# Kernel optimization log

Hardware: AMD Instinct MI355X
Metric: run time of the kernel (lower is better)

## Reference

```python
import jax, jax.numpy as jnp
import numpy as np
from jax import lax

DIM = 512
DH = 16          # dim_head
H = DIM // DH    # 32 heads
WS = 7           # window_size
SR = 3           # sr_ratio (AvgPool2d kernel, stride=1)
EPS = 1e-5


def _rel_pos_indices():
    # mirrors the torch buffer construction, incl. the [:, 24:] slice for sr_ratio>1
    pos = np.arange(WS)
    gi, gj = np.meshgrid(pos, pos, indexing='ij')
    grid = np.stack([gi, gj], axis=-1).reshape(-1, 2)            # (49, 2)
    rel = grid[:, None, :] - grid[None, :, :] + (WS - 1)         # (49, 49, 2)
    idx = rel[..., 0] * (2 * WS - 1) + rel[..., 1]               # (49, 49)
    return jnp.asarray(idx[:, 24:], dtype=jnp.int32)             # (49, 25)


def _layernorm(x, g, b):
    m = jnp.mean(x, axis=-1, keepdims=True)
    v = jnp.mean(jnp.square(x - m), axis=-1, keepdims=True)
    return (x - m) * lax.rsqrt(v + EPS) * g + b


def setup_inputs() -> dict:
    key = jax.random.key(0)
    ks = jax.random.split(key, 8)
    B, X, Y = 8, 14, 14
    x = jax.random.normal(ks[0], (B, X, Y, WS, WS, DIM), dtype=jnp.float32)
    ln_gamma = 1.0 + 0.1 * jax.random.normal(ks[1], (DIM,), dtype=jnp.float32)
    ln_beta = 0.1 * jax.random.normal(ks[2], (DIM,), dtype=jnp.float32)
    s = 1.0 / np.sqrt(DIM)
    Wq = jax.random.normal(ks[3], (DIM, DIM), dtype=jnp.float32) * s
    Wkv = jax.random.normal(ks[4], (2 * DIM, DIM), dtype=jnp.float32) * s
    Wout = jax.random.normal(ks[5], (DIM, DIM), dtype=jnp.float32) * s
    rel_pos_emb = 0.02 * jax.random.normal(ks[6], ((2 * WS - 1) ** 2, H), dtype=jnp.float32)
    return {"x": x, "ln_gamma": ln_gamma, "ln_beta": ln_beta,
            "Wq": Wq, "Wkv": Wkv, "Wout": Wout, "rel_pos_emb": rel_pos_emb}


def reference(x, ln_gamma, ln_beta, Wq, Wkv, Wout, rel_pos_emb):
    B, X, Y, W1, W2, D = x.shape
    Nw = B * X * Y                      # number of windows
    Nq = W1 * W2                        # 49 query tokens per window
    xn = _layernorm(x, ln_gamma, ln_beta)
    xw = xn.reshape(Nw, Nq, D)
    # queries
    q = (xw @ Wq.T).reshape(Nw, Nq, H, DH).transpose(0, 2, 1, 3) * (DH ** -0.5)  # (Nw,H,Nq,DH)
    # KV spatial reduction: AvgPool2d(kernel=SR, stride=1) over the 7x7 window
    xi = xw.reshape(Nw, W1, W2, D)
    xp = lax.reduce_window(xi, 0.0, lax.add, (1, SR, SR, 1), (1, 1, 1, 1), 'VALID') / (SR * SR)
    Hp, Wp = W1 - SR + 1, W2 - SR + 1   # 5, 5
    xkv = _layernorm(xp.reshape(Nw, Hp * Wp, D), ln_gamma, ln_beta)
    # to_kv with einops '(dim h l)' decomposition: last axis factored as (DH, H, 2)
    kv = (xkv @ Wkv.T).reshape(Nw, Hp * Wp, DH, H, 2)
    k = kv[..., 0].transpose(0, 3, 1, 2)  # (Nw, H, Nk, DH)
    v = kv[..., 1].transpose(0, 3, 1, 2)
    sim = jnp.einsum('bhid,bhjd->bhij', q, k)                    # (Nw,H,49,25)
    bias = rel_pos_emb[_rel_pos_indices()]                       # (49,25,H)
    sim = sim + bias.transpose(2, 0, 1)[None]
    attn = jax.nn.softmax(sim, axis=-1)
    out = jnp.einsum('bhij,bhjd->bhid', attn, v)                 # (Nw,H,49,DH)
    out = out.reshape(Nw, H, W1, W2, DH).transpose(0, 2, 3, 1, 4).reshape(Nw, W1, W2, D)
    out = out @ Wout.T
    return out.reshape(B, X, Y, W1, W2, D)
```

## Files before the change

### kernel.cpp

```cpp
#include <hip/hip_runtime.h>

typedef _Float16 half8 __attribute__((ext_vector_type(8)));
typedef _Float16 half4 __attribute__((ext_vector_type(4)));
typedef float f32x4 __attribute__((ext_vector_type(4)));

#define MFMA16(a,b,c) __builtin_amdgcn_mfma_f32_16x16x32_f16(a,b,c,0,0,0)
#define GLOAD16(g, l) __builtin_amdgcn_global_load_lds( \
  (const __attribute__((address_space(1))) void*)(g), \
  (__attribute__((address_space(3))) void*)(l), 16, 0, 0)
#define SCHEDB() __builtin_amdgcn_sched_barrier(0)

static constexpr int NW     = 1568;
static constexpr int MROWSQ = 76832;
static constexpr int MPADQ  = 76928;
static constexpr int MROWKV = 39200;
static constexpr int MPADKV = 39296;
static constexpr float LOG2E = 1.4426950408889634f;

__device__ __forceinline__ half8 h8z(){
  half8 z = {(_Float16)0,(_Float16)0,(_Float16)0,(_Float16)0,
             (_Float16)0,(_Float16)0,(_Float16)0,(_Float16)0};
  return z;
}

__global__ void k_prep_w(const float* __restrict__ a, const float* __restrict__ b,
                         const float* __restrict__ c,
                         _Float16* __restrict__ ah, _Float16* __restrict__ bh,
                         _Float16* __restrict__ ch){
  int i = blockIdx.x*256 + threadIdx.x;
  if(i < 262144) ah[i] = (_Float16)(a[i]*(0.25f*LOG2E));
  int j = i - 262144;
  if(j >= 0 && j < 524288) bh[j] = (_Float16)b[j];
  int k = i - 786432;
  if(k >= 0 && k < 262144) ch[k] = (_Float16)c[k];
}

__global__ void k_prep_bias(const float* __restrict__ rel, float* __restrict__ biasT){
  int t = blockIdx.x*256 + threadIdx.x;
  if(t >= 65536) return;
  int h = t >> 11;
  int r = t & 2047;
  int i = r >> 5, slotk = r & 31;
  int kg = slotk >> 3, idx = slotk & 7;
  int j = (idx < 4) ? (kg*4 + idx) : (16 + kg*4 + idx - 4);
  float v = 0.f;
  if(j >= 25) v = -1e30f;
  else if(i < 49){
    int qi = i/7, qj = i%7;
    int c = j + 24, ki = c/7, kj = c%7;
    v = rel[((qi-ki+6)*13 + (qj-kj+6))*32 + h];
  }
  biasT[t] = v*LOG2E;
}

__global__ __launch_bounds__(512) void k_ln_pool(const float* __restrict__ x,
    const float* __restrict__ gamma, const float* __restrict__ beta,
    _Float16* __restrict__ xn, _Float16* __restrict__ xkv){
  __shared__ _Float16 nrm[49*512];
  const int w = blockIdx.x, t = threadIdx.x;
  const int lane = t & 63, wv = t >> 6;
  float gf[8], bf[8];
  {
    float4 g0 = *(const float4*)(gamma + lane*8);
    float4 g1 = *(const float4*)(gamma + lane*8 + 4);
    float4 b0 = *(const float4*)(beta  + lane*8);
    float4 b1 = *(const float4*)(beta  + lane*8 + 4);
    gf[0]=g0.x; gf[1]=g0.y; gf[2]=g0.z; gf[3]=g0.w;
    gf[4]=g1.x; gf[5]=g1.y; gf[6]=g1.z; gf[7]=g1.w;
    bf[0]=b0.x; bf[1]=b0.y; bf[2]=b0.z; bf[3]=b0.w;
    bf[4]=b1.x; bf[5]=b1.y; bf[6]=b1.z; bf[7]=b1.w;
  }
  const float* xw = x + (size_t)w*49*512;
  for(int i = wv; i < 49; i += 8){
    const float* row = xw + i*512 + lane*8;
    float4 v0 = *(const float4*)row;
    float4 v1 = *(const float4*)(row+4);
    float v[8] = {v0.x,v0.y,v0.z,v0.w,v1.x,v1.y,v1.z,v1.w};
    float s = 0.f, sq = 0.f;
    #pragma unroll
    for(int j=0;j<8;j++){ s += v[j]; sq += v[j]*v[j]; }
    #pragma unroll
    for(int o=32;o>=1;o>>=1){ s += __shfl_xor(s,o); sq += __shfl_xor(sq,o); }
    float mean = s*(1.f/512.f);
    float rstd = rsqrtf(sq*(1.f/512.f) - mean*mean + 1e-5f);
    half8 nh;
    #pragma unroll
    for(int j=0;j<8;j++)
      nh[j] = (_Float16)((v[j]-mean)*rstd*gf[j] + bf[j]);
    *(half8*)&nrm[i*512 + lane*8] = nh;
    *(half8*)(xn + ((size_t)w*49 + i)*512 + lane*8) = nh;
  }
  __syncthreads();
  for(int p = wv; p < 25; p += 8){
    const int pi = p/5, pj = p%5;
    float acc[8] = {0,0,0,0,0,0,0,0};
    #pragma unroll
    for(int a=0;a<3;a++)
      #pragma unroll
      for(int bb=0;bb<3;bb++){
        half8 rv = *(const half8*)&nrm[((pi+a)*7 + (pj+bb))*512 + lane*8];
        #pragma unroll
        for(int j=0;j<8;j++) acc[j] += (float)rv[j];
      }
    float s = 0.f, sq = 0.f;
    #pragma unroll
    for(int j=0;j<8;j++){ acc[j] *= (1.f/9.f); s += acc[j]; sq += acc[j]*acc[j]; }
    #pragma unroll
    for(int o=32;o>=1;o>>=1){ s += __shfl_xor(s,o); sq += __shfl_xor(sq,o); }
    float mean = s*(1.f/512.f);
    float rstd = rsqrtf(sq*(1.f/512.f) - mean*mean + 1e-5f);
    half8 nh;
    #pragma unroll
    for(int j=0;j<8;j++) nh[j] = (_Float16)((acc[j]-mean)*rstd*gf[j] + bf[j]);
    *(half8*)(xkv + ((size_t)w*25 + p)*512 + lane*8) = nh;
  }
}

template<int MODE>
__global__ __launch_bounds__(256) void k_gemm(const _Float16* __restrict__ A,
    const _Float16* __restrict__ Bw, _Float16* __restrict__ oh,
    float* __restrict__ of, int ldc, int ntn, int nwg){
  __shared__ __align__(16) _Float16 As[3][128*32];
  __shared__ __align__(16) _Float16 Bs[3][128*32];
  const int orig = blockIdx.x;
  const int xcd = orig & 7, slot = orig >> 3;
  const int q8 = nwg >> 3, r8 = nwg & 7;
  const int base = (xcd < r8) ? xcd*(q8+1) : r8*(q8+1) + (xcd-r8)*q8;
  const int lin = base + slot;
  const int m0 = (lin / ntn) * 128, n0 = (lin % ntn) * 128;
  const int t = threadIdx.x, lane = t & 63;
  const int wid = t >> 6, wm = (wid>>1)*64, wn = (wid&1)*64;
  const int lr = lane & 15, kg = lane >> 4;
  const _Float16* Ab = A  + (size_t)m0*512;
  const _Float16* Bb = Bw + (size_t)n0*512;
  const int foff0 = wid*64, foff1 = 256 + wid*64;
  const int f0 = foff0 + lane, f1 = foff1 + lane;
  const int r0 = f0 >> 2, r1 = f1 >> 2;
  const size_t ga0 = (size_t)r0*512 + ((f0&3) ^ ((r0>>1)&3))*8;
  const size_t ga1 = (size_t)r1*512 + ((f1&3) ^ ((r1>>1)&3))*8;
  const int swz = (lr>>1) & 3;

  auto STAGE = [&](int buf, int kt){
    const int k0 = kt*32;
    GLOAD16(Ab + ga0 + k0, &As[buf][foff0*8]);
    GLOAD16(Bb + ga0 + k0, &Bs[buf][foff0*8]);
    GLOAD16(Ab + ga1 + k0, &As[buf][foff1*8]);
    GLOAD16(Bb + ga1 + k0, &Bs[buf][foff1*8]);
  };
  STAGE(0, 0);
  STAGE(1, 1);

  f32x4 acc[4][4] = {};
  int buf = 0;
  for(int kt = 0; kt < 16; ++kt){
    if(kt + 2 < 16){
      int nb = buf + 2; if(nb >= 3) nb -= 3;
      STAGE(nb, kt + 2);
    }
    if(kt < 14)       asm volatile("s_waitcnt vmcnt(8)" ::: "memory");
    else if(kt == 14) asm volatile("s_waitcnt vmcnt(4)" ::: "memory");
    else              asm volatile("s_waitcnt vmcnt(0)" ::: "memory");
    SCHEDB();
    __builtin_amdgcn_s_barrier();
    SCHEDB();
    const _Float16* Ac = As[buf];
    const _Float16* Bc = Bs[buf];
    half8 af[4], bf[4];
    #pragma unroll
    for(int mt=0;mt<4;mt++)
      af[mt] = *(const half8*)&Ac[(wm + mt*16 + lr)*32 + (kg ^ swz)*8];
    #pragma unroll
    for(int nt=0;nt<4;nt++)
      bf[nt] = *(const half8*)&Bc[(wn + nt*16 + lr)*32 + (kg ^ swz)*8];
    #pragma unroll
    for(int mt=0;mt<4;mt++)
      #pragma unroll
      for(int nt=0;nt<4;nt++)
        acc[mt][nt] = MFMA16(af[mt], bf[nt], acc[mt][nt]);
    SCHEDB();
    __builtin_amdgcn_s_barrier();
    SCHEDB();
    buf += 1; if(buf >= 3) buf -= 3;
  }
  #pragma unroll
  for(int mt=0;mt<4;mt++)
    #pragma unroll
    for(int nt=0;nt<4;nt++)
      #pragma unroll
      for(int r=0;r<4;r++){
        int row = m0 + wm + mt*16 + kg*4 + r;
        int col = n0 + wn + nt*16 + lr;
        float vv = acc[mt][nt][r];
        if(MODE == 0){
          oh[(size_t)row*ldc + col] = (_Float16)vv;
        } else {
          if(row < MROWSQ) of[(size_t)row*ldc + col] = vv;
        }
      }
}

__global__ __launch_bounds__(256) void k_repack(const _Float16* __restrict__ kvb,
    _Float16* __restrict__ kb, _Float16* __restrict__ vb){
  __shared__ uint2 s2[6400];
  uint32_t* su = (uint32_t*)s2;
  const int w = blockIdx.x, t = threadIdx.x;
  const uint2* src = (const uint2*)(kvb + (size_t)w*25*1024);
  #pragma unroll
  for(int it=0; it<25; ++it){
    int U = it*256 + t;
    int j = U >> 8, u = U & 255;
    s2[j*256 + (u ^ (u>>4) ^ (j&15))] = src[U];
  }
  __syncthreads();
  _Float16* kdst = kb + (size_t)w*12800;
  for(int it=0; it<7; ++it){
    int q = it*256 + t;
    if(q < 1600){
      int h = q/50, rem = q%50, j = rem>>1, half = rem&1;
      half8 k8;
      #pragma unroll
      for(int jj=0;jj<8;jj++){
        int dh = half*8 + jj;
        int slot = j*256 + ((dh*16 + (h>>1)) ^ dh ^ (j&15));
        uint32_t val = su[slot*2 + (h&1)];
        k8[jj] = ((_Float16*)&val)[0];
      }
      *(half8*)(kdst + q*8) = k8;
    }
  }
  _Float16* vtdst = vb + (size_t)w*16384;
  for(int it=0; it<8; ++it){
    int u = it*256 + t;
    int h = u >> 6, rem = u & 63;
    int dh = rem >> 2, jq = rem & 3;
    half8 v8 = h8z();
    #pragma unroll
    for(int jj=0;jj<8;jj++){
      int j = jq*8 + jj;
      if(j < 25){
        int slot = j*256 + ((dh*16 + (h>>1)) ^ dh ^ (j&15));
        uint32_t val = su[slot*2 + (h&1)];
        v8[jj] = ((_Float16*)&val)[1];
      }
    }
    *(half8*)(vtdst + u*8) = v8;
  }
}

__global__ __launch_bounds__(256) void k_attn(const _Float16* __restrict__ q,
    const _Float16* __restrict__ kb, const _Float16* __restrict__ vb,
    const float* __restrict__ biasT, _Float16* __restrict__ ao){
  const int w = blockIdx.x, hi = blockIdx.y, t = threadIdx.x;
  const int lane = t & 63, wv = t >> 6;
  const int lr = lane & 15, kg = lane >> 4;
  const size_t qbase = ((size_t)w*49)*512;
  const int hA = hi*4 + wv;
  const size_t kvA = (((size_t)w*32 + hA)*25)*16;
  const size_t kvB = kvA + 6400;
  half8 kA0=h8z(), kA1=h8z(), kB0=h8z(), kB1=h8z();
  if(kg < 2){
    kA0 = *(const half8*)(kb + kvA + lr*16 + kg*8);
    kB0 = *(const half8*)(kb + kvB + lr*16 + kg*8);
    if(lr < 9){
      kA1 = *(const half8*)(kb + kvA + (16+lr)*16 + kg*8);
      kB1 = *(const half8*)(kb + kvB + (16+lr)*16 + kg*8);
    }
  }
  half8 qA[4], qB[4];
  #pragma unroll
  for(int qt=0;qt<4;qt++){
    if(kg < 2){
      const _Float16* p = q + qbase + (size_t)(qt*16+lr)*512 + hA*16 + kg*8;
      qA[qt] = *(const half8*)p;
      qB[qt] = *(const half8*)(p + 256);
    } else { qA[qt] = h8z(); qB[qt] = h8z(); }
  }
  half8 vA, vB;
  {
    const _Float16* vtA = vb + ((size_t)w*32 + hA)*512 + lr*32 + kg*4;
    const _Float16* vtB = vtA + 16*512;
    half4 a0 = *(const half4*)vtA;
    half4 a1 = *(const half4*)(vtA + 16);
    half4 b0 = *(const half4*)vtB;
    half4 b1 = *(const half4*)(vtB + 16);
    vA = __builtin_shufflevector(a0, a1, 0,1,2,3,4,5,6,7);
    vB = __builtin_shufflevector(b0, b1, 0,1,2,3,4,5,6,7);
  }
  const float4* btA = (const float4*)(biasT + (size_t)hA*2048);
  const float4* btB = (const float4*)(biasT + (size_t)(hA+16)*2048);
  #pragma unroll
  for(int qt=0;qt<4;qt++){
    f32x4 sA0={}, sA1={}, sB0={}, sB1={};
    sA0 = MFMA16(kA0, qA[qt], sA0);
    sA1 = MFMA16(kA1, qA[qt], sA1);
    sB0 = MFMA16(kB0, qB[qt], sB0);
    sB1 = MFMA16(kB1, qB[qt], sB1);
    const int i = qt*16 + lr;
    const int bidx = i*8 + kg*2;
    float4 bA0 = btA[bidx], bA1 = btA[bidx+1];
    float4 bB0 = btB[bidx], bB1 = btB[bidx+1];
    float a[8], b[8];
    a[0]=sA0[0]+bA0.x; a[1]=sA0[1]+bA0.y; a[2]=sA0[2]+bA0.z; a[3]=sA0[3]+bA0.w;
    a[4]=sA1[0]+bA1.x; a[5]=sA1[1]+bA1.y; a[6]=sA1[2]+bA1.z; a[7]=sA1[3]+bA1.w;
    b[0]=sB0[0]+bB0.x; b[1]=sB0[1]+bB0.y; b[2]=sB0[2]+bB0.z; b[3]=sB0[3]+bB0.w;
    b[4]=sB1[0]+bB1.x; b[5]=sB1[1]+bB1.y; b[6]=sB1[2]+bB1.z; b[7]=sB1[3]+bB1.w;
    float mA = a[0], mB = b[0];
    #pragma unroll
    for(int j=1;j<8;j++){ mA = fmaxf(mA, a[j]); mB = fmaxf(mB, b[j]); }
    mA = fmaxf(mA, __shfl_xor(mA,16)); mB = fmaxf(mB, __shfl_xor(mB,16));
    mA = fmaxf(mA, __shfl_xor(mA,32)); mB = fmaxf(mB, __shfl_xor(mB,32));
    float sumA = 0.f, sumB = 0.f;
    #pragma unroll
    for(int j=0;j<8;j++){
      a[j] = exp2f(a[j]-mA); sumA += a[j];
      b[j] = exp2f(b[j]-mB); sumB += b[j];
    }
    sumA += __shfl_xor(sumA,16); sumB += __shfl_xor(sumB,16);
    sumA += __shfl_xor(sumA,32); sumB += __shfl_xor(sumB,32);
    float invA = 1.f/sumA, invB = 1.f/sumB;
    half8 pA, pB;
    #pragma unroll
    for(int j=0;j<8;j++){
      pA[j] = (_Float16)(a[j]*invA);
      pB[j] = (_Float16)(b[j]*invB);
    }
    f32x4 oA={}, oB={};
    oA = MFMA16(pA, vA, oA);
    oB = MFMA16(pB, vB, oB);
    #pragma unroll
    for(int r=0;r<4;r++){
      int qi2 = qt*16 + kg*4 + r;
      if(qi2 < 49){
        _Float16* dst = ao + qbase + (size_t)qi2*512 + hA*16 + lr;
        dst[0]   = (_Float16)oA[r];
        dst[256] = (_Float16)oB[r];
      }
    }
  }
}

extern "C" void kernel_launch(void* const* d_in, const int* in_sizes, int n_in,
                              void* d_out, int out_size, void* d_ws, size_t ws_size,
                              hipStream_t stream){
  (void)in_sizes; (void)n_in; (void)out_size; (void)ws_size;
  const float* x    = (const float*)d_in[0];
  const float* gam  = (const float*)d_in[1];
  const float* bet  = (const float*)d_in[2];
  const float* Wq   = (const float*)d_in[3];
  const float* Wkv  = (const float*)d_in[4];
  const float* Wout = (const float*)d_in[5];
  const float* rel  = (const float*)d_in[6];
  float* out = (float*)d_out;

  char* ws = (char*)d_ws;
  size_t off = 0;
  auto alloc = [&](size_t n){ char* p = ws + off; off += (n + 1023) & ~(size_t)1023; return p; };
  _Float16* xn    = (_Float16*)alloc((size_t)MPADQ*512*2);
  _Float16* xkv   = (_Float16*)alloc((size_t)MPADKV*512*2);
  _Float16* kvb   = (_Float16*)alloc((size_t)MPADKV*1024*2);
  _Float16* kbuf  = (_Float16*)alloc((size_t)NW*32*25*16*2);
  _Float16* vbuf  = (_Float16*)alloc((size_t)NW*32*16*32*2);
  _Float16* wqh   = (_Float16*)alloc((size_t)262144*2);
  _Float16* wkvh  = (_Float16*)alloc((size_t)524288*2);
  _Float16* wouth = (_Float16*)alloc((size_t)262144*2);
  float*    biasT = (float*)   alloc((size_t)65536*4);
  _Float16* qb    = kvb;

  k_prep_w   <<<dim3(4096), 256, 0, stream>>>(Wq, Wkv, Wout, wqh, wkvh, wouth);
  k_prep_bias<<<dim3(256),  256, 0, stream>>>(rel, biasT);
  k_ln_pool  <<<dim3(NW),   512, 0, stream>>>(x, gam, bet, xn, xkv);
  k_gemm<0>  <<<dim3(2456), 256, 0, stream>>>(xkv, wkvh, kvb, nullptr, 1024, 8, 2456);
  k_repack   <<<dim3(NW),   256, 0, stream>>>(kvb, kbuf, vbuf);
  k_gemm<0>  <<<dim3(2404), 256, 0, stream>>>(xn,  wqh,  qb,  nullptr,  512, 4, 2404);
  k_attn     <<<dim3(NW,4), 256, 0, stream>>>(qb, kbuf, vbuf, biasT, xn);
  k_gemm<1>  <<<dim3(2404), 256, 0, stream>>>(xn,  wouth, nullptr, out, 512, 4, 2404);
}
```

Baseline: 385.5 us.

## Process four heads per wave in attention and two rows per iteration in LN

The attention kernel now has each wave handle four heads (strided by 8) instead of two, which halves the grid's y dimension. Q fragments are loaded per query tile inside the loop rather than all being preloaded. The LN/pool kernel processes two rows or pooled positions per wave iteration to expose more independent memory loads and shuffle reductions. These changes aim to raise instruction-level parallelism and amortise per-block overhead, at the cost of more registers and fewer blocks.

```diff
diff --git a/kernel.cpp b/kernel.cpp
--- a/kernel.cpp
+++ b/kernel.cpp
@@ -71,48 +71,102 @@
     bf[4]=b1.x; bf[5]=b1.y; bf[6]=b1.z; bf[7]=b1.w;
   }
   const float* xw = x + (size_t)w*49*512;
-  for(int i = wv; i < 49; i += 8){
-    const float* row = xw + i*512 + lane*8;
-    float4 v0 = *(const float4*)row;
-    float4 v1 = *(const float4*)(row+4);
-    float v[8] = {v0.x,v0.y,v0.z,v0.w,v1.x,v1.y,v1.z,v1.w};
-    float s = 0.f, sq = 0.f;
-    #pragma unroll
-    for(int j=0;j<8;j++){ s += v[j]; sq += v[j]*v[j]; }
-    #pragma unroll
-    for(int o=32;o>=1;o>>=1){ s += __shfl_xor(s,o); sq += __shfl_xor(sq,o); }
-    float mean = s*(1.f/512.f);
-    float rstd = rsqrtf(sq*(1.f/512.f) - mean*mean + 1e-5f);
-    half8 nh;
-    #pragma unroll
-    for(int j=0;j<8;j++)
-      nh[j] = (_Float16)((v[j]-mean)*rstd*gf[j] + bf[j]);
-    *(half8*)&nrm[i*512 + lane*8] = nh;
-    *(half8*)(xn + ((size_t)w*49 + i)*512 + lane*8) = nh;
+  for(int i0 = wv; i0 < 49; i0 += 16){
+    const int i1 = i0 + 8;
+    const bool two = (i1 < 49);
+    float v0[8], v1[8];
+    {
+      const float* r0 = xw + i0*512 + lane*8;
+      float4 a0 = *(const float4*)r0, a1 = *(const float4*)(r0+4);
+      v0[0]=a0.x; v0[1]=a0.y; v0[2]=a0.z; v0[3]=a0.w;
+      v0[4]=a1.x; v0[5]=a1.y; v0[6]=a1.z; v0[7]=a1.w;
+    }
+    if(two){
+      const float* r1 = xw + i1*512 + lane*8;
+      float4 a0 = *(const float4*)r1, a1 = *(const float4*)(r1+4);
+      v1[0]=a0.x; v1[1]=a0.y; v1[2]=a0.z; v1[3]=a0.w;
+      v1[4]=a1.x; v1[5]=a1.y; v1[6]=a1.z; v1[7]=a1.w;
+    } else {
+      #pragma unroll
+      for(int j=0;j<8;j++) v1[j] = 0.f;
+    }
+    float s0=0.f, q0=0.f, s1=0.f, q1=0.f;
+    #pragma unroll
+    for(int j=0;j<8;j++){
+      s0 += v0[j]; q0 += v0[j]*v0[j];
+      s1 += v1[j]; q1 += v1[j]*v1[j];
+    }
+    #pragma unroll
+    for(int o=32;o>=1;o>>=1){
+      s0 += __shfl_xor(s0,o); q0 += __shfl_xor(q0,o);
+      s1 += __shfl_xor(s1,o); q1 += __shfl_xor(q1,o);
+    }
+    float m0 = s0*(1.f/512.f), m1 = s1*(1.f/512.f);
+    float r0 = rsqrtf(q0*(1.f/512.f) - m0*m0 + 1e-5f);
+    float r1 = rsqrtf(q1*(1.f/512.f) - m1*m1 + 1e-5f);
+    half8 n0, n1;
+    #pragma unroll
+    for(int j=0;j<8;j++){
+      n0[j] = (_Float16)((v0[j]-m0)*r0*gf[j] + bf[j]);
+      n1[j] = (_Float16)((v1[j]-m1)*r1*gf[j] + bf[j]);
+    }
+    *(half8*)&nrm[i0*512 + lane*8] = n0;
+    *(half8*)(xn + ((size_t)w*49 + i0)*512 + lane*8) = n0;
+    if(two){
+      *(half8*)&nrm[i1*512 + lane*8] = n1;
+      *(half8*)(xn + ((size_t)w*49 + i1)*512 + lane*8) = n1;
+    }
   }
   __syncthreads();
-  for(int p = wv; p < 25; p += 8){
-    const int pi = p/5, pj = p%5;
-    float acc[8] = {0,0,0,0,0,0,0,0};
-    #pragma unroll
-    for(int a=0;a<3;a++)
-      #pragma unroll
-      for(int bb=0;bb<3;bb++){
-        half8 rv = *(const half8*)&nrm[((pi+a)*7 + (pj+bb))*512 + lane*8];
+  for(int p0 = wv; p0 < 25; p0 += 16){
+    const int p1 = p0 + 8;
+    const bool two = (p1 < 25);
+    float ac0[8] = {0,0,0,0,0,0,0,0}, ac1[8] = {0,0,0,0,0,0,0,0};
+    {
+      const int pi = p0/5, pj = p0%5;
+      #pragma unroll
+      for(int a=0;a<3;a++)
         #pragma unroll
-        for(int j=0;j<8;j++) acc[j] += (float)rv[j];
-      }
-    float s = 0.f, sq = 0.f;
-    #pragma unroll
-    for(int j=0;j<8;j++){ acc[j] *= (1.f/9.f); s += acc[j]; sq += acc[j]*acc[j]; }
-    #pragma unroll
-    for(int o=32;o>=1;o>>=1){ s += __shfl_xor(s,o); sq += __shfl_xor(sq,o); }
-    float mean = s*(1.f/512.f);
-    float rstd = rsqrtf(sq*(1.f/512.f) - mean*mean + 1e-5f);
-    half8 nh;
-    #pragma unroll
-    for(int j=0;j<8;j++) nh[j] = (_Float16)((acc[j]-mean)*rstd*gf[j] + bf[j]);
-    *(half8*)(xkv + ((size_t)w*25 + p)*512 + lane*8) = nh;
+        for(int bb=0;bb<3;bb++){
+          half8 rv = *(const half8*)&nrm[((pi+a)*7 + (pj+bb))*512 + lane*8];
+          #pragma unroll
+          for(int j=0;j<8;j++) ac0[j] += (float)rv[j];
+        }
+    }
+    if(two){
+      const int pi = p1/5, pj = p1%5;
+      #pragma unroll
+      for(int a=0;a<3;a++)
+        #pragma unroll
+        for(int bb=0;bb<3;bb++){
+          half8 rv = *(const half8*)&nrm[((pi+a)*7 + (pj+bb))*512 + lane*8];
+          #pragma unroll
+          for(int j=0;j<8;j++) ac1[j] += (float)rv[j];
+        }
+    }
+    float s0=0.f, q0=0.f, s1=0.f, q1=0.f;
+    #pragma unroll
+    for(int j=0;j<8;j++){
+      ac0[j] *= (1.f/9.f); s0 += ac0[j]; q0 += ac0[j]*ac0[j];
+      ac1[j] *= (1.f/9.f); s1 += ac1[j]; q1 += ac1[j]*ac1[j];
+    }
+    #pragma unroll
+    for(int o=32;o>=1;o>>=1){
+      s0 += __shfl_xor(s0,o); q0 += __shfl_xor(q0,o);
+      s1 += __shfl_xor(s1,o); q1 += __shfl_xor(q1,o);
+    }
+    float m0 = s0*(1.f/512.f), m1 = s1*(1.f/512.f);
+    float r0 = rsqrtf(q0*(1.f/512.f) - m0*m0 + 1e-5f);
+    float r1 = rsqrtf(q1*(1.f/512.f) - m1*m1 + 1e-5f);
+    half8 n0, n1;
+    #pragma unroll
+    for(int j=0;j<8;j++){
+      n0[j] = (_Float16)((ac0[j]-m0)*r0*gf[j] + bf[j]);
+      n1[j] = (_Float16)((ac1[j]-m1)*r1*gf[j] + bf[j]);
+    }
+    *(half8*)(xkv + ((size_t)w*25 + p0)*512 + lane*8) = n0;
+    if(two)
+      *(half8*)(xkv + ((size_t)w*25 + p1)*512 + lane*8) = n1;
   }
 }
 
@@ -254,86 +308,68 @@
   const int lane = t & 63, wv = t >> 6;
   const int lr = lane & 15, kg = lane >> 4;
   const size_t qbase = ((size_t)w*49)*512;
-  const int hA = hi*4 + wv;
-  const size_t kvA = (((size_t)w*32 + hA)*25)*16;
-  const size_t kvB = kvA + 6400;
-  half8 kA0=h8z(), kA1=h8z(), kB0=h8z(), kB1=h8z();
-  if(kg < 2){
-    kA0 = *(const half8*)(kb + kvA + lr*16 + kg*8);
-    kB0 = *(const half8*)(kb + kvB + lr*16 + kg*8);
-    if(lr < 9){
-      kA1 = *(const half8*)(kb + kvA + (16+lr)*16 + kg*8);
-      kB1 = *(const half8*)(kb + kvB + (16+lr)*16 + kg*8);
-    }
-  }
-  half8 qA[4], qB[4];
+  const int hbase = hi*4 + wv;
+  half8 k0[4], k1[4], vf[4];
   #pragma unroll
-  for(int qt=0;qt<4;qt++){
+  for(int c=0;c<4;c++){
+    const int h = hbase + c*8;
+    const size_t kvh = (((size_t)w*32 + h)*25)*16;
+    k0[c] = h8z(); k1[c] = h8z();
     if(kg < 2){
-      const _Float16* p = q + qbase + (size_t)(qt*16+lr)*512 + hA*16 + kg*8;
-      qA[qt] = *(const half8*)p;
-      qB[qt] = *(const half8*)(p + 256);
-    } else { qA[qt] = h8z(); qB[qt] = h8z(); }
-  }
-  half8 vA, vB;
-  {
-    const _Float16* vtA = vb + ((size_t)w*32 + hA)*512 + lr*32 + kg*4;
-    const _Float16* vtB = vtA + 16*512;
-    half4 a0 = *(const half4*)vtA;
-    half4 a1 = *(const half4*)(vtA + 16);
-    half4 b0 = *(const half4*)vtB;
-    half4 b1 = *(const half4*)(vtB + 16);
-    vA = __builtin_shufflevector(a0, a1, 0,1,2,3,4,5,6,7);
-    vB = __builtin_shufflevector(b0, b1, 0,1,2,3,4,5,6,7);
-  }
-  const float4* btA = (const float4*)(biasT + (size_t)hA*2048);
-  const float4* btB = (const float4*)(biasT + (size_t)(hA+16)*2048);
-  #pragma unroll
-  for(int qt=0;qt<4;qt++){
-    f32x4 sA0={}, sA1={}, sB0={}, sB1={};
-    sA0 = MFMA16(kA0, qA[qt], sA0);
-    sA1 = MFMA16(kA1, qA[qt], sA1);
-    sB0 = MFMA16(kB0, qB[qt], sB0);
-    sB1 = MFMA16(kB1, qB[qt], sB1);
+      k0[c] = *(const half8*)(kb + kvh + lr*16 + kg*8);
+      if(lr < 9) k1[c] = *(const half8*)(kb + kvh + (16+lr)*16 + kg*8);
+    }
+    const _Float16* vt = vb + ((size_t)w*32 + h)*512 + lr*32 + kg*4;
+    half4 a0 = *(const half4*)vt;
+    half4 a1 = *(const half4*)(vt + 16);
+    vf[c] = __builtin_shufflevector(a0, a1, 0,1,2,3,4,5,6,7);
+  }
+  for(int qt=0; qt<4; qt++){
+    half8 qf[4];
+    #pragma unroll
+    for(int c=0;c<4;c++){
+      if(kg < 2){
+        qf[c] = *(const half8*)(q + qbase + (size_t)(qt*16+lr)*512
+                                + (hbase + c*8)*16 + kg*8);
+      } else qf[c] = h8z();
+    }
+    f32x4 s0[4], s1[4];
+    #pragma unroll
+    for(int c=0;c<4;c++){
+      f32x4 z0={}, z1={};
+      s0[c] = MFMA16(k0[c], qf[c], z0);
+      s1[c] = MFMA16(k1[c], qf[c], z1);
+    }
     const int i = qt*16 + lr;
     const int bidx = i*8 + kg*2;
-    float4 bA0 = btA[bidx], bA1 = btA[bidx+1];
-    float4 bB0 = btB[bidx], bB1 = btB[bidx+1];
-    float a[8], b[8];
-    a[0]=sA0[0]+bA0.x; a[1]=sA0[1]+bA0.y; a[2]=sA0[2]+bA0.z; a[3]=sA0[3]+bA0.w;
-    a[4]=sA1[0]+bA1.x; a[5]=sA1[1]+bA1.y; a[6]=sA1[2]+bA1.z; a[7]=sA1[3]+bA1.w;
-    b[0]=sB0[0]+bB0.x; b[1]=sB0[1]+bB0.y; b[2]=sB0[2]+bB0.z; b[3]=sB0[3]+bB0.w;
-    b[4]=sB1[0]+bB1.x; b[5]=sB1[1]+bB1.y; b[6]=sB1[2]+bB1.z; b[7]=sB1[3]+bB1.w;
-    float mA = a[0], mB = b[0];
-    #pragma unroll
-    for(int j=1;j<8;j++){ mA = fmaxf(mA, a[j]); mB = fmaxf(mB, b[j]); }
-    mA = fmaxf(mA, __shfl_xor(mA,16)); mB = fmaxf(mB, __shfl_xor(mB,16));
-    mA = fmaxf(mA, __shfl_xor(mA,32)); mB = fmaxf(mB, __shfl_xor(mB,32));
-    float sumA = 0.f, sumB = 0.f;
-    #pragma unroll
-    for(int j=0;j<8;j++){
-      a[j] = exp2f(a[j]-mA); sumA += a[j];
-      b[j] = exp2f(b[j]-mB); sumB += b[j];
-    }
-    sumA += __shfl_xor(sumA,16); sumB += __shfl_xor(sumB,16);
-    sumA += __shfl_xor(sumA,32); sumB += __shfl_xor(sumB,32);
-    float invA = 1.f/sumA, invB = 1.f/sumB;
-    half8 pA, pB;
-    #pragma unroll
-    for(int j=0;j<8;j++){
-      pA[j] = (_Float16)(a[j]*invA);
-      pB[j] = (_Float16)(b[j]*invB);
-    }
-    f32x4 oA={}, oB={};
-    oA = MFMA16(pA, vA, oA);
-    oB = MFMA16(pB, vB, oB);
-    #pragma unroll
-    for(int r=0;r<4;r++){
-      int qi2 = qt*16 + kg*4 + r;
-      if(qi2 < 49){
-        _Float16* dst = ao + qbase + (size_t)qi2*512 + hA*16 + lr;
-        dst[0]   = (_Float16)oA[r];
-        dst[256] = (_Float16)oB[r];
+    #pragma unroll
+    for(int c=0;c<4;c++){
+      const float4* bt = (const float4*)(biasT + (size_t)(hbase + c*8)*2048);
+      float4 b0 = bt[bidx], b1 = bt[bidx+1];
+      float a[8];
+      a[0]=s0[c][0]+b0.x; a[1]=s0[c][1]+b0.y; a[2]=s0[c][2]+b0.z; a[3]=s0[c][3]+b0.w;
+      a[4]=s1[c][0]+b1.x; a[5]=s1[c][1]+b1.y; a[6]=s1[c][2]+b1.z; a[7]=s1[c][3]+b1.w;
+      float m = a[0];
+      #pragma unroll
+      for(int j=1;j<8;j++) m = fmaxf(m, a[j]);
+      m = fmaxf(m, __shfl_xor(m,16));
+      m = fmaxf(m, __shfl_xor(m,32));
+      float sum = 0.f;
+      #pragma unroll
+      for(int j=0;j<8;j++){ a[j] = exp2f(a[j]-m); sum += a[j]; }
+      sum += __shfl_xor(sum,16);
+      sum += __shfl_xor(sum,32);
+      float inv = 1.f/sum;
+      half8 p8;
+      #pragma unroll
+      for(int j=0;j<8;j++) p8[j] = (_Float16)(a[j]*inv);
+      f32x4 o = {};
+      o = MFMA16(p8, vf[c], o);
+      #pragma unroll
+      for(int r=0;r<4;r++){
+        int qi2 = qt*16 + kg*4 + r;
+        if(qi2 < 49)
+          ao[qbase + (size_t)qi2*512 + (hbase + c*8)*16 + lr] = (_Float16)o[r];
       }
     }
   }
@@ -372,6 +408,6 @@
   k_gemm<0>  <<<dim3(2456), 256, 0, stream>>>(xkv, wkvh, kvb, nullptr, 1024, 8, 2456);
   k_repack   <<<dim3(NW),   256, 0, stream>>>(kvb, kbuf, vbuf);
   k_gemm<0>  <<<dim3(2404), 256, 0, stream>>>(xn,  wqh,  qb,  nullptr,  512, 4, 2404);
-  k_attn     <<<dim3(NW,4), 256, 0, stream>>>(qb, kbuf, vbuf, biasT, xn);
+  k_attn     <<<dim3(NW,2), 256, 0, stream>>>(qb, kbuf, vbuf, biasT, xn);
   k_gemm<1>  <<<dim3(2404), 256, 0, stream>>>(xn,  wouth, nullptr, out, 512, 4, 2404);
 }
```

Measured after the change: 412.4 us. 7.0% more time.
